# Kernel tuning notes

Measured on AMD Instinct MI355X. Metric: run time of the kernel, lower is better.

Reference implementation:

```python
import jax, jax.numpy as jnp
import numpy as np

N_EVENT, N_IOC = 10000, 40000
N = N_EVENT + N_IOC
E = 800000
D_EVENT, D_IOC = 768, 128
H = 256            # hidden_dim
R = 8              # num_relations
B = 8              # num_bases
L = 3              # num_layers
EDIM = 16          # edge_type_embed_dim
LN_EPS = 1e-5


def setup_inputs() -> dict:
    key = jax.random.key(0)
    ks = jax.random.split(key, 24)
    inp = {}
    inp['x_event'] = jax.random.normal(ks[0], (N_EVENT, D_EVENT), dtype=jnp.float32)
    inp['x_ioc'] = jax.random.normal(ks[1], (N_IOC, D_IOC), dtype=jnp.float32)
    inp['edge_index'] = jax.random.randint(ks[2], (2, E), 0, N, dtype=jnp.int32)
    inp['edge_type'] = jax.random.randint(ks[3], (E,), 0, R, dtype=jnp.int32)
    inp['edge_weight'] = jax.random.uniform(ks[4], (E,), dtype=jnp.float32)
    # input projection params (Linear + LayerNorm per node type)
    inp['proj_event_w'] = jax.random.normal(ks[5], (D_EVENT, H), dtype=jnp.float32) / np.sqrt(D_EVENT)
    inp['proj_event_b'] = jnp.zeros((H,), jnp.float32)
    inp['proj_event_g'] = jnp.ones((H,), jnp.float32)
    inp['proj_event_beta'] = jnp.zeros((H,), jnp.float32)
    inp['proj_ioc_w'] = jax.random.normal(ks[6], (D_IOC, H), dtype=jnp.float32) / np.sqrt(D_IOC)
    inp['proj_ioc_b'] = jnp.zeros((H,), jnp.float32)
    inp['proj_ioc_g'] = jnp.ones((H,), jnp.float32)
    inp['proj_ioc_beta'] = jnp.zeros((H,), jnp.float32)
    # edge-type embedding + edge MLP
    inp['edge_emb'] = jax.random.normal(ks[7], (R, EDIM), dtype=jnp.float32)
    inp['edge_mlp_w'] = jax.random.normal(ks[8], (EDIM + 1, H), dtype=jnp.float32) / np.sqrt(EDIM + 1)
    inp['edge_mlp_b'] = jnp.zeros((H,), jnp.float32)
    # RGCN layers: basis-decomposed relation weights + root + bias, per-layer LayerNorm
    inp['conv_bases'] = jax.random.normal(ks[9], (L, B, H, H), dtype=jnp.float32) / np.sqrt(H)
    inp['conv_comp'] = jax.random.normal(ks[10], (L, R, B), dtype=jnp.float32) / np.sqrt(B)
    inp['conv_root'] = jax.random.normal(ks[11], (L, H, H), dtype=jnp.float32) / np.sqrt(H)
    inp['conv_bias'] = jnp.zeros((L, H), jnp.float32)
    inp['norm_gamma'] = jnp.ones((L, H), jnp.float32)
    inp['norm_beta'] = jnp.zeros((L, H), jnp.float32)
    return inp


def _ln(x, g, b):
    mu = jnp.mean(x, axis=-1, keepdims=True)
    var = jnp.var(x, axis=-1, keepdims=True)
    return (x - mu) * jax.lax.rsqrt(var + LN_EPS) * g + b


def reference(x_event, x_ioc, edge_index, edge_type, edge_weight,
              proj_event_w, proj_event_b, proj_event_g, proj_event_beta,
              proj_ioc_w, proj_ioc_b, proj_ioc_g, proj_ioc_beta,
              edge_emb, edge_mlp_w, edge_mlp_b,
              conv_bases, conv_comp, conv_root, conv_bias,
              norm_gamma, norm_beta):
    # input projections: Linear -> LayerNorm -> ReLU, then concat EVENT first
    h_ev = jax.nn.relu(_ln(x_event @ proj_event_w + proj_event_b, proj_event_g, proj_event_beta))
    h_io = jax.nn.relu(_ln(x_ioc @ proj_ioc_w + proj_ioc_b, proj_ioc_g, proj_ioc_beta))
    h = jnp.concatenate([h_ev, h_io], axis=0)  # [N, H]
    n, d = h.shape
    src, dst = edge_index[0], edge_index[1]
    r = edge_emb.shape[0]

    # edge-feature MLP (edge_type embedding ++ weight), eval mode so dropout is identity
    ef = jnp.concatenate([edge_emb[edge_type], edge_weight[:, None]], axis=-1)  # [E, EDIM+1]
    enh = jax.nn.relu(ef @ edge_mlp_w + edge_mlp_b)                              # [E, H]
    enh_sum = jax.ops.segment_sum(enh, dst, num_segments=n)
    deg = jax.ops.segment_sum(jnp.ones(enh.shape[0], h.dtype), dst, num_segments=n)
    enh_mean = enh_sum / jnp.maximum(deg, 1.0)[:, None]                           # [N, H]

    ones_e = jnp.ones(src.shape[0], h.dtype)
    seg = dst.astype(jnp.int32) * r + edge_type                                   # per-(dst, relation) segments
    cnt = jnp.maximum(jax.ops.segment_sum(ones_e, seg, num_segments=n * r), 1.0)

    for l in range(conv_bases.shape[0]):
        # basis-decomposed relation weights: W_r = sum_b comp[r,b] * basis_b
        w = jnp.einsum('rb,bio->rio', conv_comp[l], conv_bases[l])   # [R, H, H]
        xr = jnp.einsum('ni,rio->rno', h, w)                          # [R, N, H]
        msg = xr[edge_type, src]                                      # [E, H]
        # per-relation mean aggregation per destination node (PyG RGCNConv aggr='mean')
        sums = jax.ops.segment_sum(msg, seg, num_segments=n * r)      # [N*R, H]
        agg = (sums / cnt[:, None]).reshape(n, r, d).sum(axis=1)      # [N, H]
        h_new = agg + h @ conv_root[l] + conv_bias[l] + 0.1 * enh_mean
        h_new = jax.nn.relu(_ln(h_new, norm_gamma[l], norm_beta[l]))
        h = h_new + h

    return h[:x_event.shape[0]]  # EVENT node embeddings
```

## Files before the change

### kernel.cpp

```cpp
#include <hip/hip_runtime.h>
#include <hip/hip_bf16.h>

#define N_EVENT 10000
#define N_IOC   40000
#define N_NODES 50000
#define E_EDGES 800000
#define D_EV 768
#define D_IO 128
#define H 256
#define R 8
#define NBASES 8
#define NLAYERS 3
#define EDIM 16
#define LN_EPS 1e-5f

#define NKEY (N_NODES * R)
#define SCAN_CHUNK 2048
#define NCHUNK ((NKEY + SCAN_CHUNK - 1) / SCAN_CHUNK)
#define NC 25000
#define NCHUNKS (N_NODES / NC)
#define KPRE (R * H)
#define KTOT (R * H + H)
#define NBEV32 ((N_EVENT + 31) / 32)
#define NBIO32 (N_IOC / 32)

typedef __hip_bfloat16 bf16;
typedef __attribute__((ext_vector_type(8))) short bf16x8;
typedef __attribute__((ext_vector_type(4))) float f32x4;

__device__ __forceinline__ float us2f(unsigned short u) {
    union { unsigned int i; float f; } x; x.i = ((unsigned int)u) << 16; return x.f;
}

__global__ __launch_bounds__(256) void hist_kernel(const int* __restrict__ ei, const int* __restrict__ et,
                                                   int* __restrict__ cnt) {
    int e = blockIdx.x * 256 + threadIdx.x;
    if (e < E_EDGES) atomicAdd(&cnt[ei[E_EDGES + e] * R + et[e]], 1);
}

__global__ __launch_bounds__(256) void scan1_kernel(const int* __restrict__ cnt, int* __restrict__ offs,
                                                    int* __restrict__ bsum) {
    __shared__ int s[256];
    int t = threadIdx.x;
    long base = (long)blockIdx.x * SCAN_CHUNK + t * 8;
    int v[8]; int sum = 0;
    #pragma unroll
    for (int i = 0; i < 8; ++i) { long idx = base + i; v[i] = (idx < NKEY) ? cnt[idx] : 0; sum += v[i]; }
    s[t] = sum; __syncthreads();
    for (int off = 1; off < 256; off <<= 1) {
        int x = (t >= off) ? s[t - off] : 0;
        __syncthreads();
        s[t] += x;
        __syncthreads();
    }
    int run = s[t] - sum;
    if (t == 255) bsum[blockIdx.x] = s[255];
    #pragma unroll
    for (int i = 0; i < 8; ++i) { long idx = base + i; if (idx < NKEY) offs[idx] = run; run += v[i]; }
}

__global__ __launch_bounds__(256) void scan2_kernel(int* __restrict__ bsum) {
    __shared__ int s[256];
    int t = threadIdx.x;
    int v = (t < NCHUNK) ? bsum[t] : 0;
    s[t] = v; __syncthreads();
    for (int off = 1; off < 256; off <<= 1) {
        int x = (t >= off) ? s[t - off] : 0;
        __syncthreads();
        s[t] += x;
        __syncthreads();
    }
    if (t < NCHUNK) bsum[t] = s[t] - v;
}

__global__ __launch_bounds__(256) void scan3_kernel(int* __restrict__ offs, const int* __restrict__ bsum) {
    int i = blockIdx.x * 256 + threadIdx.x;
    if (i < NKEY) offs[i] += bsum[i / SCAN_CHUNK];
    if (i == 0) offs[NKEY] = E_EDGES;
}

__global__ __launch_bounds__(256) void cinv_kernel(const int* __restrict__ cnt, float* __restrict__ cinv) {
    int i = blockIdx.x * 256 + threadIdx.x;
    if (i < NKEY) cinv[i] = 1.0f / (float)max(cnt[i], 1);
}

__global__ __launch_bounds__(256) void sort_kernel(const int* __restrict__ ei, const int* __restrict__ et,
                                                   const float* __restrict__ ew, const int* __restrict__ offs,
                                                   int* __restrict__ cnt, int* __restrict__ ssrc,
                                                   float* __restrict__ sew) {
    int e = blockIdx.x * 256 + threadIdx.x;
    if (e >= E_EDGES) return;
    int key = ei[E_EDGES + e] * R + et[e];
    int pos = offs[key] + atomicSub(&cnt[key], 1) - 1;
    ssrc[pos] = ei[e];
    sew[pos]  = ew[e];
}

__global__ __launch_bounds__(256) void cvt_x_kernel(const float* __restrict__ xev, const float* __restrict__ xio,
                                                    bf16* __restrict__ xevb, bf16* __restrict__ xiob) {
    const long NEV4 = (long)N_EVENT * D_EV / 4;
    const long NTOT4 = NEV4 + (long)N_IOC * D_IO / 4;
    long i = (long)blockIdx.x * 256 + threadIdx.x;
    if (i >= NTOT4) return;
    const float4* src; ushort4* dst; long j;
    if (i < NEV4) { src = (const float4*)xev; dst = (ushort4*)xevb; j = i; }
    else          { src = (const float4*)xio; dst = (ushort4*)xiob; j = i - NEV4; }
    float4 v = src[j];
    ushort4 o;
    bf16 a0 = __float2bfloat16(v.x), a1 = __float2bfloat16(v.y);
    bf16 a2 = __float2bfloat16(v.z), a3 = __float2bfloat16(v.w);
    o.x = *(unsigned short*)&a0; o.y = *(unsigned short*)&a1;
    o.z = *(unsigned short*)&a2; o.w = *(unsigned short*)&a3;
    dst[j] = o;
}

__global__ __launch_bounds__(256) void cvt_w_kernel(const float* __restrict__ wev, const float* __restrict__ wio,
                                                    bf16* __restrict__ wevT, bf16* __restrict__ wioT) {
    int n = blockIdx.x;
    for (int k = threadIdx.x; k < D_EV; k += 256)
        wevT[(size_t)n * D_EV + k] = __float2bfloat16(wev[(size_t)k * H + n]);
    for (int k = threadIdx.x; k < D_IO; k += 256)
        wioT[(size_t)n * D_IO + k] = __float2bfloat16(wio[(size_t)k * H + n]);
}

__global__ __launch_bounds__(256) void build_Bt_kernel(
    const float* __restrict__ bases, const float* __restrict__ comp, const float* __restrict__ root,
    bf16* __restrict__ Bt3) {
    int gb = blockIdx.x;
    int l = gb / KTOT, krow = gb % KTOT;
    int n = threadIdx.x;
    float v;
    if (krow < KPRE) {
        int r = krow >> 8, kk = krow & 255;
        v = 0.0f;
        const float* bs = bases + (size_t)l * NBASES * H * H + (size_t)kk * H + n;
        const float* cp = comp + (l * R + r) * NBASES;
        #pragma unroll
        for (int b = 0; b < NBASES; ++b) v += cp[b] * bs[(size_t)b * H * H];
    } else {
        int kk = krow - KPRE;
        v = root[((size_t)l * H + kk) * H + n];
    }
    Bt3[(size_t)l * H * KTOT + (size_t)n * KTOT + krow] = __float2bfloat16(v);
}

__global__ __launch_bounds__(256) void edge_table_kernel(
    const float* __restrict__ emb, const float* __restrict__ mlp_w,
    const float* __restrict__ mlp_b, float* __restrict__ ctab, float* __restrict__ wlast) {
    int r = blockIdx.x, j = threadIdx.x;
    float acc = mlp_b[j];
    #pragma unroll
    for (int k = 0; k < EDIM; ++k) acc += emb[r * EDIM + k] * mlp_w[k * H + j];
    ctab[r * H + j] = acc;
    if (r == 0) wlast[j] = mlp_w[EDIM * H + j];
}

__global__ __launch_bounds__(256) void enh_bucket_kernel(
    const int* __restrict__ offs, const float* __restrict__ sew,
    const float* __restrict__ ctab, const float* __restrict__ wlast,
    bf16* __restrict__ enh) {
    __shared__ float ct[R * H];
    __shared__ float wl[H];
    for (int i = threadIdx.x; i < R * H; i += 256) ct[i] = ctab[i];
    for (int i = threadIdx.x; i < H; i += 256) wl[i] = wlast[i];
    __syncthreads();
    int w = threadIdx.x >> 6, lane = threadIdx.x & 63;
    int d = blockIdx.x * 4 + w;
    float acc[4] = {0.f, 0.f, 0.f, 0.f};
    int deg = offs[d * R + R] - offs[d * R];
    for (int r = 0; r < R; ++r) {
        int a = offs[d * R + r], b = offs[d * R + r + 1];
        for (int j = a; j < b; ++j) {
            float wt = sew[j];
            #pragma unroll
            for (int i = 0; i < 4; ++i) {
                int c = lane * 4 + i;
                acc[i] += fmaxf(ct[r * H + c] + wt * wl[c], 0.0f);
            }
        }
    }
    float inv = 1.0f / fmaxf((float)deg, 1.0f);
    unsigned short o[4];
    #pragma unroll
    for (int i = 0; i < 4; ++i) { bf16 hv = __float2bfloat16(acc[i] * inv); o[i] = *(unsigned short*)&hv; }
    *(ushort4*)(enh + (size_t)d * H + lane * 4) = *(ushort4*)o;
}

__global__ __launch_bounds__(256) void bucket_msg_kernel(
    const int* __restrict__ offs, const int* __restrict__ ssrc,
    const bf16* __restrict__ hbR, const float* __restrict__ cinv,
    bf16* __restrict__ pre, int c0) {
    int w = threadIdx.x >> 6, lane = threadIdx.x & 63;
    int d = c0 + blockIdx.x;
    size_t prow = (size_t)blockIdx.x * KPRE;
    #pragma unroll
    for (int rr = 0; rr < 2; ++rr) {
        int r = w * 2 + rr;
        float acc[4] = {0.f, 0.f, 0.f, 0.f};
        int a = offs[d * R + r], b = offs[d * R + r + 1];
        for (int j = a; j < b; ++j) {
            int s = ssrc[j];
            ushort4 u = *(const ushort4*)(hbR + (size_t)s * H + lane * 4);
            acc[0] += us2f(u.x); acc[1] += us2f(u.y); acc[2] += us2f(u.z); acc[3] += us2f(u.w);
        }
        float sc = cinv[d * R + r];
        unsigned short o[4];
        #pragma unroll
        for (int i = 0; i < 4; ++i) { bf16 hv = __float2bfloat16(acc[i] * sc); o[i] = *(unsigned short*)&hv; }
        *(ushort4*)(pre + prow + r * H + lane * 4) = *(ushort4*)o;
    }
}

__global__ __launch_bounds__(256) void gemm3_kernel(
    const bf16* __restrict__ pre, const bf16* __restrict__ hbR,
    const bf16* __restrict__ Bt, const bf16* __restrict__ enh,
    const float* __restrict__ bias, const float* __restrict__ gamma, const float* __restrict__ beta,
    bf16* __restrict__ hbW, int c0) {
    int t = threadIdx.x, w = t >> 6, lane = t & 63;
    int quad = lane >> 4, m = lane & 15;
    int row0 = blockIdx.x * 32;
    f32x4 acc0[4], acc1[4];
    #pragma unroll
    for (int c = 0; c < 4; ++c) {
        acc0[c][0]=0.f; acc0[c][1]=0.f; acc0[c][2]=0.f; acc0[c][3]=0.f;
        acc1[c][0]=0.f; acc1[c][1]=0.f; acc1[c][2]=0.f; acc1[c][3]=0.f;
    }
    int rA0 = row0 + m;      if (rA0 >= NC) rA0 = NC - 1;
    int rA1 = row0 + 16 + m; if (rA1 >= NC) rA1 = NC - 1;
    const bf16* A0p = pre + (size_t)rA0 * KPRE;
    const bf16* A1p = pre + (size_t)rA1 * KPRE;
    const bf16* A0h = hbR + (size_t)(c0 + rA0) * H;
    const bf16* A1h = hbR + (size_t)(c0 + rA1) * H;
    const bf16* Bbase = Bt + (size_t)(w * 64 + m) * KTOT;

    for (int kc = 0; kc < KTOT / 32; ++kc) {
        int k0 = kc * 32;
        bf16x8 a0, a1;
        if (k0 < KPRE) {
            a0 = *(const bf16x8*)(A0p + k0 + quad * 8);
            a1 = *(const bf16x8*)(A1p + k0 + quad * 8);
        } else {
            a0 = *(const bf16x8*)(A0h + (k0 - KPRE) + quad * 8);
            a1 = *(const bf16x8*)(A1h + (k0 - KPRE) + quad * 8);
        }
        const bf16* bp = Bbase + k0 + quad * 8;
        #pragma unroll
        for (int c = 0; c < 4; ++c) {
            bf16x8 b = *(const bf16x8*)(bp + (size_t)c * 16 * KTOT);
            acc0[c] = __builtin_amdgcn_mfma_f32_16x16x32_bf16(a0, b, acc0[c], 0, 0, 0);
            acc1[c] = __builtin_amdgcn_mfma_f32_16x16x32_bf16(a1, b, acc1[c], 0, 0, 0);
        }
    }

    float bv[4], gv[4], tv[4];
    #pragma unroll
    for (int c = 0; c < 4; ++c) {
        int col = w * 64 + c * 16 + m;
        bv[c] = bias[col]; gv[c] = gamma[col]; tv[c] = beta[col];
    }
    float s0[4]={0,0,0,0}, q0[4]={0,0,0,0}, s1[4]={0,0,0,0}, q1[4]={0,0,0,0};
    #pragma unroll
    for (int c = 0; c < 4; ++c) {
        #pragma unroll
        for (int i = 0; i < 4; ++i) {
            int r0 = row0 + quad * 4 + i;        int rr0 = (r0 < NC) ? r0 : (NC - 1);
            int r1 = row0 + 16 + quad * 4 + i;   int rr1 = (r1 < NC) ? r1 : (NC - 1);
            int col = w * 64 + c * 16 + m;
            float e0 = us2f(*(const unsigned short*)(enh + (size_t)(c0 + rr0) * H + col));
            float e1 = us2f(*(const unsigned short*)(enh + (size_t)(c0 + rr1) * H + col));
            float v0 = acc0[c][i] + bv[c] + 0.1f * e0;
            float v1 = acc1[c][i] + bv[c] + 0.1f * e1;
            acc0[c][i] = v0; acc1[c][i] = v1;
            s0[i] += v0; q0[i] += v0 * v0;
            s1[i] += v1; q1[i] += v1 * v1;
        }
    }
    #pragma unroll
    for (int msk = 1; msk < 16; msk <<= 1) {
        #pragma unroll
        for (int i = 0; i < 4; ++i) {
            s0[i] += __shfl_xor(s0[i], msk); q0[i] += __shfl_xor(q0[i], msk);
            s1[i] += __shfl_xor(s1[i], msk); q1[i] += __shfl_xor(q1[i], msk);
        }
    }
    __shared__ float sred[4][32];
    __shared__ float qred[4][32];
    if (m == 0) {
        #pragma unroll
        for (int i = 0; i < 4; ++i) {
            sred[w][quad * 4 + i] = s0[i];      qred[w][quad * 4 + i] = q0[i];
            sred[w][16 + quad * 4 + i] = s1[i]; qred[w][16 + quad * 4 + i] = q1[i];
        }
    }
    __syncthreads();
    float mu0[4], rs0[4], mu1[4], rs1[4];
    #pragma unroll
    for (int i = 0; i < 4; ++i) {
        int rl0 = quad * 4 + i, rl1 = 16 + quad * 4 + i;
        float S0 = sred[0][rl0] + sred[1][rl0] + sred[2][rl0] + sred[3][rl0];
        float Q0 = qred[0][rl0] + qred[1][rl0] + qred[2][rl0] + qred[3][rl0];
        float S1 = sred[0][rl1] + sred[1][rl1] + sred[2][rl1] + sred[3][rl1];
        float Q1 = qred[0][rl1] + qred[1][rl1] + qred[2][rl1] + qred[3][rl1];
        mu0[i] = S0 * (1.0f / H);
        rs0[i] = rsqrtf(Q0 * (1.0f / H) - mu0[i] * mu0[i] + LN_EPS);
        mu1[i] = S1 * (1.0f / H);
        rs1[i] = rsqrtf(Q1 * (1.0f / H) - mu1[i] * mu1[i] + LN_EPS);
    }
    #pragma unroll
    for (int c = 0; c < 4; ++c) {
        #pragma unroll
        for (int i = 0; i < 4; ++i) {
            int col = w * 64 + c * 16 + m;
            int r0 = row0 + quad * 4 + i;
            if (r0 < NC) {
                size_t idx = (size_t)(c0 + r0) * H + col;
                float y = (acc0[c][i] - mu0[i]) * rs0[i] * gv[c] + tv[c];
                float hn = us2f(*(const unsigned short*)(hbR + idx)) + fmaxf(y, 0.0f);
                hbW[idx] = __float2bfloat16(hn);
            }
            int r1 = row0 + 16 + quad * 4 + i;
            if (r1 < NC) {
                size_t idx = (size_t)(c0 + r1) * H + col;
                float y = (acc1[c][i] - mu1[i]) * rs1[i] * gv[c] + tv[c];
                float hn = us2f(*(const unsigned short*)(hbR + idx)) + fmaxf(y, 0.0f);
                hbW[idx] = __float2bfloat16(hn);
            }
        }
    }
}

__global__ __launch_bounds__(256) void proj3_kernel(
    const bf16* __restrict__ xevb, const bf16* __restrict__ xiob,
    const bf16* __restrict__ wevT, const bf16* __restrict__ wioT,
    const float* __restrict__ bev, const float* __restrict__ gev, const float* __restrict__ betev,
    const float* __restrict__ bio, const float* __restrict__ gio, const float* __restrict__ betio,
    bf16* __restrict__ hbW) {
    int t = threadIdx.x, w = t >> 6, lane = t & 63;
    int quad = lane >> 4, m = lane & 15;
    int blk = blockIdx.x;
    const bf16 *X, *WT; const float *bb, *gg, *be;
    int K, node0, x0, nvalid;
    if (blk < NBEV32) {
        X = xevb; WT = wevT; K = D_EV; x0 = blk * 32; node0 = x0;
        bb = bev; gg = gev; be = betev;
        nvalid = (N_EVENT - x0 < 32) ? (N_EVENT - x0) : 32;
    } else {
        int b2 = blk - NBEV32;
        X = xiob; WT = wioT; K = D_IO; x0 = b2 * 32; node0 = N_EVENT + x0;
        bb = bio; gg = gio; be = betio;
        nvalid = 32;
    }
    f32x4 acc0[4], acc1[4];
    #pragma unroll
    for (int c = 0; c < 4; ++c) {
        acc0[c][0]=0.f; acc0[c][1]=0.f; acc0[c][2]=0.f; acc0[c][3]=0.f;
        acc1[c][0]=0.f; acc1[c][1]=0.f; acc1[c][2]=0.f; acc1[c][3]=0.f;
    }
    int rA0 = m;      if (rA0 >= nvalid) rA0 = nvalid - 1;
    int rA1 = 16 + m; if (rA1 >= nvalid) rA1 = nvalid - 1;
    const bf16* A0 = X + (size_t)(x0 + rA0) * K;
    const bf16* A1 = X + (size_t)(x0 + rA1) * K;
    const bf16* Bbase = WT + (size_t)(w * 64 + m) * K;

    for (int kc = 0; kc < K / 32; ++kc) {
        int k0 = kc * 32;
        bf16x8 a0 = *(const bf16x8*)(A0 + k0 + quad * 8);
        bf16x8 a1 = *(const bf16x8*)(A1 + k0 + quad * 8);
        const bf16* bp = Bbase + k0 + quad * 8;
        #pragma unroll
        for (int c = 0; c < 4; ++c) {
            bf16x8 b = *(const bf16x8*)(bp + (size_t)c * 16 * K);
            acc0[c] = __builtin_amdgcn_mfma_f32_16x16x32_bf16(a0, b, acc0[c], 0, 0, 0);
            acc1[c] = __builtin_amdgcn_mfma_f32_16x16x32_bf16(a1, b, acc1[c], 0, 0, 0);
        }
    }

    float bv[4], gv[4], tv[4];
    #pragma unroll
    for (int c = 0; c < 4; ++c) {
        int col = w * 64 + c * 16 + m;
        bv[c] = bb[col]; gv[c] = gg[col]; tv[c] = be[col];
    }
    float s0[4]={0,0,0,0}, q0[4]={0,0,0,0}, s1[4]={0,0,0,0}, q1[4]={0,0,0,0};
    #pragma unroll
    for (int c = 0; c < 4; ++c) {
        #pragma unroll
        for (int i = 0; i < 4; ++i) {
            float v0 = acc0[c][i] + bv[c];
            float v1 = acc1[c][i] + bv[c];
            acc0[c][i] = v0; acc1[c][i] = v1;
            s0[i] += v0; q0[i] += v0 * v0;
            s1[i] += v1; q1[i] += v1 * v1;
        }
    }
    #pragma unroll
    for (int msk = 1; msk < 16; msk <<= 1) {
        #pragma unroll
        for (int i = 0; i < 4; ++i) {
            s0[i] += __shfl_xor(s0[i], msk); q0[i] += __shfl_xor(q0[i], msk);
            s1[i] += __shfl_xor(s1[i], msk); q1[i] += __shfl_xor(q1[i], msk);
        }
    }
    __shared__ float sred[4][32];
    __shared__ float qred[4][32];
    if (m == 0) {
        #pragma unroll
        for (int i = 0; i < 4; ++i) {
            sred[w][quad * 4 + i] = s0[i];      qred[w][quad * 4 + i] = q0[i];
            sred[w][16 + quad * 4 + i] = s1[i]; qred[w][16 + quad * 4 + i] = q1[i];
        }
    }
    __syncthreads();
    float mu0[4], rs0[4], mu1[4], rs1[4];
    #pragma unroll
    for (int i = 0; i < 4; ++i) {
        int rl0 = quad * 4 + i, rl1 = 16 + quad * 4 + i;
        float S0 = sred[0][rl0] + sred[1][rl0] + sred[2][rl0] + sred[3][rl0];
        float Q0 = qred[0][rl0] + qred[1][rl0] + qred[2][rl0] + qred[3][rl0];
        float S1 = sred[0][rl1] + sred[1][rl1] + sred[2][rl1] + sred[3][rl1];
        float Q1 = qred[0][rl1] + qred[1][rl1] + qred[2][rl1] + qred[3][rl1];
        mu0[i] = S0 * (1.0f / H);
        rs0[i] = rsqrtf(Q0 * (1.0f / H) - mu0[i] * mu0[i] + LN_EPS);
        mu1[i] = S1 * (1.0f / H);
        rs1[i] = rsqrtf(Q1 * (1.0f / H) - mu1[i] * mu1[i] + LN_EPS);
    }
    #pragma unroll
    for (int c = 0; c < 4; ++c) {
        #pragma unroll
        for (int i = 0; i < 4; ++i) {
            int col = w * 64 + c * 16 + m;
            int r0 = quad * 4 + i;
            if (r0 < nvalid) {
                float y = (acc0[c][i] - mu0[i]) * rs0[i] * gv[c] + tv[c];
                hbW[(size_t)(node0 + r0) * H + col] = __float2bfloat16(fmaxf(y, 0.0f));
            }
            int r1 = 16 + quad * 4 + i;
            if (r1 < nvalid) {
                float y = (acc1[c][i] - mu1[i]) * rs1[i] * gv[c] + tv[c];
                hbW[(size_t)(node0 + r1) * H + col] = __float2bfloat16(fmaxf(y, 0.0f));
            }
        }
    }
}

__global__ __launch_bounds__(256) void out_kernel(const bf16* __restrict__ hb, float* __restrict__ out) {
    size_t i = (size_t)blockIdx.x * 256 + threadIdx.x;
    if (i < (size_t)N_EVENT * H) out[i] = us2f(*(const unsigned short*)(hb + i));
}

extern "C" void kernel_launch(void* const* d_in, const int* in_sizes, int n_in,
                              void* d_out, int out_size, void* d_ws, size_t ws_size,
                              hipStream_t stream) {
    const float* xev   = (const float*)d_in[0];
    const float* xio   = (const float*)d_in[1];
    const int*   ei    = (const int*)d_in[2];
    const int*   et    = (const int*)d_in[3];
    const float* ew    = (const float*)d_in[4];
    const float* wev   = (const float*)d_in[5];
    const float* bev   = (const float*)d_in[6];
    const float* gev   = (const float*)d_in[7];
    const float* betev = (const float*)d_in[8];
    const float* wio   = (const float*)d_in[9];
    const float* bio   = (const float*)d_in[10];
    const float* gio   = (const float*)d_in[11];
    const float* betio = (const float*)d_in[12];
    const float* emb   = (const float*)d_in[13];
    const float* mlp_w = (const float*)d_in[14];
    const float* mlp_b = (const float*)d_in[15];
    const float* bases = (const float*)d_in[16];
    const float* comp  = (const float*)d_in[17];
    const float* root  = (const float*)d_in[18];
    const float* bias  = (const float*)d_in[19];
    const float* gamma = (const float*)d_in[20];
    const float* beta  = (const float*)d_in[21];

    char* base = (char*)d_ws;
    size_t o = 0;
    auto alloc = [&](size_t bytes) { char* p = base + o; o = (o + bytes + 255) & ~(size_t)255; return p; };
    bf16*  hbA  = (bf16*) alloc((size_t)N_NODES * H * 2);
    bf16*  hbB  = (bf16*) alloc((size_t)N_NODES * H * 2);
    bf16*  enh  = (bf16*) alloc((size_t)N_NODES * H * 2);
    char*  un   = alloc((size_t)NC * KPRE * 2);
    bf16*  pre  = (bf16*)un;
    bf16*  xevb = (bf16*)un;
    bf16*  xiob = (bf16*)(un + (size_t)N_EVENT * D_EV * 2);
    bf16*  wevT = (bf16*) alloc((size_t)H * D_EV * 2);
    bf16*  wioT = (bf16*) alloc((size_t)H * D_IO * 2);
    bf16*  Bt3  = (bf16*) alloc((size_t)NLAYERS * H * KTOT * 2);
    float* ctab = (float*)alloc(R * H * 4);
    float* wlast= (float*)alloc(H * 4);
    float* cinv = (float*)alloc((size_t)NKEY * 4);
    int*   bsum = (int*)  alloc(256 * 4);
    int*   cnt  = (int*)  alloc((size_t)NKEY * 4);
    int*   offs = (int*)  alloc((size_t)(NKEY + 4) * 4);
    int*   ssrc = (int*)  alloc((size_t)E_EDGES * 4);
    float* sew  = (float*)alloc((size_t)E_EDGES * 4);

    hipMemsetAsync(cnt, 0, (size_t)NKEY * sizeof(int), stream);

    hist_kernel<<<(E_EDGES + 255) / 256, 256, 0, stream>>>(ei, et, cnt);
    scan1_kernel<<<NCHUNK, 256, 0, stream>>>(cnt, offs, bsum);
    scan2_kernel<<<1, 256, 0, stream>>>(bsum);
    scan3_kernel<<<(NKEY + 255) / 256, 256, 0, stream>>>(offs, bsum);
    cinv_kernel<<<(NKEY + 255) / 256, 256, 0, stream>>>(cnt, cinv);
    sort_kernel<<<(E_EDGES + 255) / 256, 256, 0, stream>>>(ei, et, ew, offs, cnt, ssrc, sew);

    cvt_x_kernel<<<12500, 256, 0, stream>>>(xev, xio, xevb, xiob);
    cvt_w_kernel<<<H, 256, 0, stream>>>(wev, wio, wevT, wioT);
    build_Bt_kernel<<<NLAYERS * KTOT, 256, 0, stream>>>(bases, comp, root, Bt3);

    proj3_kernel<<<NBEV32 + NBIO32, 256, 0, stream>>>(
        xevb, xiob, wevT, wioT, bev, gev, betev, bio, gio, betio, hbA);
    edge_table_kernel<<<R, 256, 0, stream>>>(emb, mlp_w, mlp_b, ctab, wlast);
    enh_bucket_kernel<<<N_NODES / 4, 256, 0, stream>>>(offs, sew, ctab, wlast, enh);

    for (int l = 0; l < NLAYERS; ++l) {
        bf16* hbR = (l & 1) ? hbB : hbA;
        bf16* hbW = (l & 1) ? hbA : hbB;
        const bf16* Bt = Bt3 + (size_t)l * H * KTOT;
        for (int c = 0; c < NCHUNKS; ++c) {
            int c0 = c * NC;
            bucket_msg_kernel<<<NC, 256, 0, stream>>>(offs, ssrc, hbR, cinv, pre, c0);
            gemm3_kernel<<<(NC + 31) / 32, 256, 0, stream>>>(
                pre, hbR, Bt, enh, bias + l * H, gamma + l * H, beta + l * H, hbW, c0);
        }
    }

    out_kernel<<<((size_t)N_EVENT * H + 255) / 256, 256, 0, stream>>>(hbB, (float*)d_out);
}
```

Before: 1.961 ms.

## Fuse per-relation gather-mean into the MFMA layer GEMM, dropping the pre buffer

Replaces the two-kernel scheme (a bucket gather that writes per-relation means to a large bf16 'pre' buffer, then a GEMM over it) with a single layer kernel. Each wave gathers the neighbour rows for its 16 destination rows directly into MFMA A-fragments on the fly, so the 2048-wide pre matrix never goes through memory, and the chunk loop collapses to one launch per layer. In exchange, each wave now computes all 256 output columns (16 accumulators), so register pressure rises. The gather is also done per lane with divergent edge-count loops inside the K loop, which may stall the MFMAs.

New measurement: 3.516 ms. +79.2%, slower.

```diff
diff --git a/kernel.cpp b/kernel.cpp
--- a/kernel.cpp
+++ b/kernel.cpp
@@ -17,12 +17,11 @@
 #define NKEY (N_NODES * R)
 #define SCAN_CHUNK 2048
 #define NCHUNK ((NKEY + SCAN_CHUNK - 1) / SCAN_CHUNK)
-#define NC 25000
-#define NCHUNKS (N_NODES / NC)
 #define KPRE (R * H)
 #define KTOT (R * H + H)
 #define NBEV32 ((N_EVENT + 31) / 32)
 #define NBIO32 (N_IOC / 32)
+#define NBLK64 ((N_NODES + 63) / 64)
 
 typedef __hip_bfloat16 bf16;
 typedef __attribute__((ext_vector_type(8))) short bf16x8;
@@ -186,142 +185,106 @@
     *(ushort4*)(enh + (size_t)d * H + lane * 4) = *(ushort4*)o;
 }
 
-__global__ __launch_bounds__(256) void bucket_msg_kernel(
-    const int* __restrict__ offs, const int* __restrict__ ssrc,
-    const bf16* __restrict__ hbR, const float* __restrict__ cinv,
-    bf16* __restrict__ pre, int c0) {
-    int w = threadIdx.x >> 6, lane = threadIdx.x & 63;
-    int d = c0 + blockIdx.x;
-    size_t prow = (size_t)blockIdx.x * KPRE;
-    #pragma unroll
-    for (int rr = 0; rr < 2; ++rr) {
-        int r = w * 2 + rr;
-        float acc[4] = {0.f, 0.f, 0.f, 0.f};
-        int a = offs[d * R + r], b = offs[d * R + r + 1];
-        for (int j = a; j < b; ++j) {
-            int s = ssrc[j];
-            ushort4 u = *(const ushort4*)(hbR + (size_t)s * H + lane * 4);
-            acc[0] += us2f(u.x); acc[1] += us2f(u.y); acc[2] += us2f(u.z); acc[3] += us2f(u.w);
-        }
-        float sc = cinv[d * R + r];
-        unsigned short o[4];
-        #pragma unroll
-        for (int i = 0; i < 4; ++i) { bf16 hv = __float2bfloat16(acc[i] * sc); o[i] = *(unsigned short*)&hv; }
-        *(ushort4*)(pre + prow + r * H + lane * 4) = *(ushort4*)o;
-    }
-}
-
-__global__ __launch_bounds__(256) void gemm3_kernel(
-    const bf16* __restrict__ pre, const bf16* __restrict__ hbR,
-    const bf16* __restrict__ Bt, const bf16* __restrict__ enh,
+__global__ __launch_bounds__(256) void layer_kernel(
+    const int* __restrict__ offs, const int* __restrict__ ssrc, const float* __restrict__ cinv,
+    const bf16* __restrict__ hbR, const bf16* __restrict__ Bt, const bf16* __restrict__ enh,
     const float* __restrict__ bias, const float* __restrict__ gamma, const float* __restrict__ beta,
-    bf16* __restrict__ hbW, int c0) {
+    bf16* __restrict__ hbW)
+{
     int t = threadIdx.x, w = t >> 6, lane = t & 63;
     int quad = lane >> 4, m = lane & 15;
-    int row0 = blockIdx.x * 32;
-    f32x4 acc0[4], acc1[4];
-    #pragma unroll
-    for (int c = 0; c < 4; ++c) {
-        acc0[c][0]=0.f; acc0[c][1]=0.f; acc0[c][2]=0.f; acc0[c][3]=0.f;
-        acc1[c][0]=0.f; acc1[c][1]=0.f; acc1[c][2]=0.f; acc1[c][3]=0.f;
-    }
-    int rA0 = row0 + m;      if (rA0 >= NC) rA0 = NC - 1;
-    int rA1 = row0 + 16 + m; if (rA1 >= NC) rA1 = NC - 1;
-    const bf16* A0p = pre + (size_t)rA0 * KPRE;
-    const bf16* A1p = pre + (size_t)rA1 * KPRE;
-    const bf16* A0h = hbR + (size_t)(c0 + rA0) * H;
-    const bf16* A1h = hbR + (size_t)(c0 + rA1) * H;
-    const bf16* Bbase = Bt + (size_t)(w * 64 + m) * KTOT;
-
-    for (int kc = 0; kc < KTOT / 32; ++kc) {
+    int row0 = blockIdx.x * 64 + w * 16;
+    int dst = row0 + m;
+    int dstc = (dst < N_NODES) ? dst : (N_NODES - 1);
+
+    f32x4 acc[16];
+    #pragma unroll
+    for (int c = 0; c < 16; ++c) { acc[c][0]=0.f; acc[c][1]=0.f; acc[c][2]=0.f; acc[c][3]=0.f; }
+
+    const bf16* Bq = Bt + (size_t)m * KTOT;
+    int bs = 0, be = 0; float sc = 0.f;
+
+    for (int kc = 0; kc < 64; ++kc) {
         int k0 = kc * 32;
-        bf16x8 a0, a1;
-        if (k0 < KPRE) {
-            a0 = *(const bf16x8*)(A0p + k0 + quad * 8);
-            a1 = *(const bf16x8*)(A1p + k0 + quad * 8);
-        } else {
-            a0 = *(const bf16x8*)(A0h + (k0 - KPRE) + quad * 8);
-            a1 = *(const bf16x8*)(A1h + (k0 - KPRE) + quad * 8);
-        }
-        const bf16* bp = Bbase + k0 + quad * 8;
-        #pragma unroll
-        for (int c = 0; c < 4; ++c) {
+        if ((kc & 7) == 0) {
+            int key = dstc * R + (kc >> 3);
+            bs = offs[key]; be = offs[key + 1]; sc = cinv[key];
+        }
+        int coff = (k0 & 255) + quad * 8;
+        float af[8] = {0.f,0.f,0.f,0.f,0.f,0.f,0.f,0.f};
+        for (int j = bs; j < be; ++j) {
+            int s = ssrc[j];
+            bf16x8 hv = *(const bf16x8*)(hbR + (size_t)s * H + coff);
+            #pragma unroll
+            for (int i = 0; i < 8; ++i) af[i] += us2f((unsigned short)hv[i]);
+        }
+        bf16x8 a;
+        #pragma unroll
+        for (int i = 0; i < 8; ++i) {
+            bf16 x = __float2bfloat16(af[i] * sc);
+            a[i] = (short)*(unsigned short*)&x;
+        }
+        const bf16* bp = Bq + k0 + quad * 8;
+        #pragma unroll
+        for (int c = 0; c < 16; ++c) {
             bf16x8 b = *(const bf16x8*)(bp + (size_t)c * 16 * KTOT);
-            acc0[c] = __builtin_amdgcn_mfma_f32_16x16x32_bf16(a0, b, acc0[c], 0, 0, 0);
-            acc1[c] = __builtin_amdgcn_mfma_f32_16x16x32_bf16(a1, b, acc1[c], 0, 0, 0);
-        }
-    }
-
-    float bv[4], gv[4], tv[4];
-    #pragma unroll
-    for (int c = 0; c < 4; ++c) {
-        int col = w * 64 + c * 16 + m;
+            acc[c] = __builtin_amdgcn_mfma_f32_16x16x32_bf16(a, b, acc[c], 0, 0, 0);
+        }
+    }
+    {
+        const bf16* Arow = hbR + (size_t)dstc * H;
+        #pragma unroll
+        for (int kc = 64; kc < 72; ++kc) {
+            int k0 = kc * 32;
+            bf16x8 a = *(const bf16x8*)(Arow + (k0 - KPRE) + quad * 8);
+            const bf16* bp = Bq + k0 + quad * 8;
+            #pragma unroll
+            for (int c = 0; c < 16; ++c) {
+                bf16x8 b = *(const bf16x8*)(bp + (size_t)c * 16 * KTOT);
+                acc[c] = __builtin_amdgcn_mfma_f32_16x16x32_bf16(a, b, acc[c], 0, 0, 0);
+            }
+        }
+    }
+
+    float bv[16], gv[16], tv[16];
+    #pragma unroll
+    for (int c = 0; c < 16; ++c) {
+        int col = c * 16 + m;
         bv[c] = bias[col]; gv[c] = gamma[col]; tv[c] = beta[col];
     }
-    float s0[4]={0,0,0,0}, q0[4]={0,0,0,0}, s1[4]={0,0,0,0}, q1[4]={0,0,0,0};
-    #pragma unroll
-    for (int c = 0; c < 4; ++c) {
-        #pragma unroll
-        for (int i = 0; i < 4; ++i) {
-            int r0 = row0 + quad * 4 + i;        int rr0 = (r0 < NC) ? r0 : (NC - 1);
-            int r1 = row0 + 16 + quad * 4 + i;   int rr1 = (r1 < NC) ? r1 : (NC - 1);
-            int col = w * 64 + c * 16 + m;
-            float e0 = us2f(*(const unsigned short*)(enh + (size_t)(c0 + rr0) * H + col));
-            float e1 = us2f(*(const unsigned short*)(enh + (size_t)(c0 + rr1) * H + col));
-            float v0 = acc0[c][i] + bv[c] + 0.1f * e0;
-            float v1 = acc1[c][i] + bv[c] + 0.1f * e1;
-            acc0[c][i] = v0; acc1[c][i] = v1;
-            s0[i] += v0; q0[i] += v0 * v0;
-            s1[i] += v1; q1[i] += v1 * v1;
+    float s[4] = {0.f,0.f,0.f,0.f}, q[4] = {0.f,0.f,0.f,0.f};
+    #pragma unroll
+    for (int c = 0; c < 16; ++c) {
+        #pragma unroll
+        for (int i = 0; i < 4; ++i) {
+            int row = row0 + quad * 4 + i;
+            int rr = (row < N_NODES) ? row : (N_NODES - 1);
+            int col = c * 16 + m;
+            float e = us2f(*(const unsigned short*)(enh + (size_t)rr * H + col));
+            float v = acc[c][i] + bv[c] + 0.1f * e;
+            acc[c][i] = v;
+            s[i] += v; q[i] += v * v;
         }
     }
     #pragma unroll
     for (int msk = 1; msk < 16; msk <<= 1) {
         #pragma unroll
-        for (int i = 0; i < 4; ++i) {
-            s0[i] += __shfl_xor(s0[i], msk); q0[i] += __shfl_xor(q0[i], msk);
-            s1[i] += __shfl_xor(s1[i], msk); q1[i] += __shfl_xor(q1[i], msk);
-        }
-    }
-    __shared__ float sred[4][32];
-    __shared__ float qred[4][32];
-    if (m == 0) {
-        #pragma unroll
-        for (int i = 0; i < 4; ++i) {
-            sred[w][quad * 4 + i] = s0[i];      qred[w][quad * 4 + i] = q0[i];
-            sred[w][16 + quad * 4 + i] = s1[i]; qred[w][16 + quad * 4 + i] = q1[i];
-        }
-    }
-    __syncthreads();
-    float mu0[4], rs0[4], mu1[4], rs1[4];
+        for (int i = 0; i < 4; ++i) { s[i] += __shfl_xor(s[i], msk); q[i] += __shfl_xor(q[i], msk); }
+    }
+    float mu[4], rs[4];
     #pragma unroll
     for (int i = 0; i < 4; ++i) {
-        int rl0 = quad * 4 + i, rl1 = 16 + quad * 4 + i;
-        float S0 = sred[0][rl0] + sred[1][rl0] + sred[2][rl0] + sred[3][rl0];
-        float Q0 = qred[0][rl0] + qred[1][rl0] + qred[2][rl0] + qred[3][rl0];
-        float S1 = sred[0][rl1] + sred[1][rl1] + sred[2][rl1] + sred[3][rl1];
-        float Q1 = qred[0][rl1] + qred[1][rl1] + qred[2][rl1] + qred[3][rl1];
-        mu0[i] = S0 * (1.0f / H);
-        rs0[i] = rsqrtf(Q0 * (1.0f / H) - mu0[i] * mu0[i] + LN_EPS);
-        mu1[i] = S1 * (1.0f / H);
-        rs1[i] = rsqrtf(Q1 * (1.0f / H) - mu1[i] * mu1[i] + LN_EPS);
-    }
-    #pragma unroll
-    for (int c = 0; c < 4; ++c) {
-        #pragma unroll
-        for (int i = 0; i < 4; ++i) {
-            int col = w * 64 + c * 16 + m;
-            int r0 = row0 + quad * 4 + i;
-            if (r0 < NC) {
-                size_t idx = (size_t)(c0 + r0) * H + col;
-                float y = (acc0[c][i] - mu0[i]) * rs0[i] * gv[c] + tv[c];
-                float hn = us2f(*(const unsigned short*)(hbR + idx)) + fmaxf(y, 0.0f);
-                hbW[idx] = __float2bfloat16(hn);
-            }
-            int r1 = row0 + 16 + quad * 4 + i;
-            if (r1 < NC) {
-                size_t idx = (size_t)(c0 + r1) * H + col;
-                float y = (acc1[c][i] - mu1[i]) * rs1[i] * gv[c] + tv[c];
+        mu[i] = s[i] * (1.0f / H);
+        rs[i] = rsqrtf(q[i] * (1.0f / H) - mu[i] * mu[i] + LN_EPS);
+    }
+    #pragma unroll
+    for (int c = 0; c < 16; ++c) {
+        #pragma unroll
+        for (int i = 0; i < 4; ++i) {
+            int row = row0 + quad * 4 + i;
+            if (row < N_NODES) {
+                size_t idx = (size_t)row * H + c * 16 + m;
+                float y = (acc[c][i] - mu[i]) * rs[i] * gv[c] + tv[c];
                 float hn = us2f(*(const unsigned short*)(hbR + idx)) + fmaxf(y, 0.0f);
                 hbW[idx] = __float2bfloat16(hn);
             }
@@ -480,10 +443,8 @@
     bf16*  hbA  = (bf16*) alloc((size_t)N_NODES * H * 2);
     bf16*  hbB  = (bf16*) alloc((size_t)N_NODES * H * 2);
     bf16*  enh  = (bf16*) alloc((size_t)N_NODES * H * 2);
-    char*  un   = alloc((size_t)NC * KPRE * 2);
-    bf16*  pre  = (bf16*)un;
-    bf16*  xevb = (bf16*)un;
-    bf16*  xiob = (bf16*)(un + (size_t)N_EVENT * D_EV * 2);
+    bf16*  xevb = (bf16*) alloc((size_t)N_EVENT * D_EV * 2);
+    bf16*  xiob = (bf16*) alloc((size_t)N_IOC * D_IO * 2);
     bf16*  wevT = (bf16*) alloc((size_t)H * D_EV * 2);
     bf16*  wioT = (bf16*) alloc((size_t)H * D_IO * 2);
     bf16*  Bt3  = (bf16*) alloc((size_t)NLAYERS * H * KTOT * 2);
@@ -517,13 +478,9 @@
     for (int l = 0; l < NLAYERS; ++l) {
         bf16* hbR = (l & 1) ? hbB : hbA;
         bf16* hbW = (l & 1) ? hbA : hbB;
-        const bf16* Bt = Bt3 + (size_t)l * H * KTOT;
-        for (int c = 0; c < NCHUNKS; ++c) {
-            int c0 = c * NC;
-            bucket_msg_kernel<<<NC, 256, 0, stream>>>(offs, ssrc, hbR, cinv, pre, c0);
-            gemm3_kernel<<<(NC + 31) / 32, 256, 0, stream>>>(
-                pre, hbR, Bt, enh, bias + l * H, gamma + l * H, beta + l * H, hbW, c0);
-        }
+        layer_kernel<<<NBLK64, 256, 0, stream>>>(
+            offs, ssrc, cinv, hbR, Bt3 + (size_t)l * H * KTOT, enh,
+            bias + l * H, gamma + l * H, beta + l * H, hbW);
     }
 
     out_kernel<<<((size_t)N_EVENT * H + 255) / 256, 256, 0, stream>>>(hbB, (float*)d_out);
```
